# Performance work log

Hardware: AMD Instinct MI355X
Metric: run time of the kernel (lower is better)

## Reference

```python
import jax, jax.numpy as jnp
import numpy as np

D_MODEL = 1024
NUM_HEADS = 16
WINDOW = 128
DEPTH = D_MODEL // NUM_HEADS


def setup_inputs() -> dict:
    key = jax.random.key(0)
    ks = jax.random.split(key, 9)
    B, S = 2, 2048
    scale = 1.0 / np.sqrt(D_MODEL)
    x = jax.random.normal(ks[0], (B, S, D_MODEL), dtype=jnp.float32)
    Wq = jax.random.normal(ks[1], (D_MODEL, D_MODEL), dtype=jnp.float32) * scale
    Wk = jax.random.normal(ks[2], (D_MODEL, D_MODEL), dtype=jnp.float32) * scale
    Wv = jax.random.normal(ks[3], (D_MODEL, D_MODEL), dtype=jnp.float32) * scale
    Wo = jax.random.normal(ks[4], (D_MODEL, D_MODEL), dtype=jnp.float32) * scale
    bq = jnp.zeros((D_MODEL,), jnp.float32)
    bk = jnp.zeros((D_MODEL,), jnp.float32)
    bv = jnp.zeros((D_MODEL,), jnp.float32)
    bo = jnp.zeros((D_MODEL,), jnp.float32)
    return {"x": x, "Wq": Wq, "bq": bq, "Wk": Wk, "bk": bk,
            "Wv": Wv, "bv": bv, "Wo": Wo, "bo": bo}


def _split_heads(t, B, S):
    # [B,S,D] -> [B,H,S,depth]
    return t.reshape(B, S, NUM_HEADS, DEPTH).transpose(0, 2, 1, 3)


def reference(x, Wq, bq, Wk, bk, Wv, bv, Wo, bo):
    B, S, _ = x.shape
    q = _split_heads(x @ Wq + bq, B, S)
    k = _split_heads(x @ Wk + bk, B, S)
    v = _split_heads(x @ Wv + bv, B, S)
    scores = jnp.einsum('bhqd,bhkd->bhqk', q, k) / jnp.sqrt(jnp.float32(DEPTH))
    idx = jnp.arange(S)
    # mask[i_row=j, i_col=i] per original: |i - j| <= window (symmetric)
    local = jnp.abs(idx[None, :] - idx[:, None]) <= WINDOW  # [S,S]
    scores = jnp.where(local[None, None], scores, jnp.float32(-1e9))
    attn = jax.nn.softmax(scores, axis=-1)
    out = jnp.einsum('bhqk,bhkd->bhqd', attn, v)
    concat = out.transpose(0, 2, 1, 3).reshape(B, S, D_MODEL)
    return concat @ Wo + bo
```

## Files before the change

kernel.cpp:

```cpp
#include <hip/hip_runtime.h>
#include <cstdint>
#include <cstddef>

typedef __attribute__((ext_vector_type(8))) short short8;
typedef __attribute__((ext_vector_type(4))) short short4v;
typedef __attribute__((ext_vector_type(4))) float f32x4;
typedef short8 bf16x8;

typedef __attribute__((address_space(1))) const unsigned GU;
typedef __attribute__((address_space(3))) unsigned LU;

__device__ __forceinline__ short f2bf(float f) {
  unsigned u = __builtin_bit_cast(unsigned, f);
  u += 0x7fffu + ((u >> 16) & 1u);
  return (short)(u >> 16);
}

__global__ __launch_bounds__(256) void k_prep(const float* __restrict__ x,
                                              const float* __restrict__ W0, const float* __restrict__ W1,
                                              const float* __restrict__ W2, const float* __restrict__ W3,
                                              short* __restrict__ xb, short* __restrict__ WT) {
  __shared__ short T[64 * 72];
  int bid = blockIdx.x;
  int tid = threadIdx.x;
  if (bid < 2048) {
    size_t i = ((size_t)bid * 256 + tid) * 8;
    f32x4 a = *(const f32x4*)(x + i);
    f32x4 b = *(const f32x4*)(x + i + 4);
    short8 o;
#pragma unroll
    for (int j = 0; j < 4; ++j) { o[j] = f2bf(a[j]); o[4 + j] = f2bf(b[j]); }
    *(short8*)(xb + i) = o;
    return;
  }
  bid -= 2048;
  int widx = bid >> 8;
  int t = bid & 255;
  int kr = (t >> 4) * 64, nc = (t & 15) * 64;
  const float* W = widx == 0 ? W0 : widx == 1 ? W1 : widx == 2 ? W2 : W3;
  short* out = WT + (size_t)widx * 1048576;
#pragma unroll
  for (int i = 0; i < 4; ++i) {
    int idx = tid + i * 256;
    int k = idx >> 4, n4 = (idx & 15) << 2;
    f32x4 v = *(const f32x4*)(W + (size_t)(kr + k) * 1024 + nc + n4);
#pragma unroll
    for (int j = 0; j < 4; ++j) T[(n4 + j) * 72 + k] = f2bf(v[j]);
  }
  __syncthreads();
#pragma unroll
  for (int i = 0; i < 2; ++i) {
    int idx = tid + i * 256;
    int n = idx >> 3, k8 = (idx & 7) << 3;
    *(short8*)(out + (size_t)(nc + n) * 1024 + kr + k8) = *(const short8*)&T[n * 72 + k8];
  }
}

__global__ __launch_bounds__(512, 1) void k_gemm256(
    const short* __restrict__ A, const short* __restrict__ BT,
    const float* __restrict__ bias0, const float* __restrict__ bias1, const float* __restrict__ bias2,
    short* __restrict__ outb) {
  __shared__ short S[73728];
  const int tid = threadIdx.x;
  const int lane = tid & 63, w = tid >> 6;
  const int g = lane >> 4, qi = lane & 15;
  const int wm = w >> 2, wn = w & 3;
  int bid = blockIdx.x;
  int xcd = bid & 7, ii = bid >> 3;
  const int tm = (xcd >> 1) * 4 + (ii >> 3);
  const int tn = (xcd & 1) * 8 + (ii & 7);
  const int m0 = tm * 256, n0 = tn * 192;
  const size_t K = 1024;
  const short* Ab = A + (size_t)m0 * K;
  const short* Bb = BT + (size_t)n0 * K;

  auto stage64 = [&](int roff, const short* gbase, int kt) {
    int r = tid >> 3;
    int js = ((tid & 7) ^ (r & 7)) << 3;
    __builtin_amdgcn_global_load_lds((GU*)(gbase + (size_t)r * K + kt * 64 + js),
                                     (LU*)(&S[roff + tid * 8]), 16, 0, 0);
  };
  auto lda_a = [&](int abase, int mf, int kk) -> bf16x8 {
    int row = (mf & 3) * 16 + qi;
    int reg = wm * 2 + (mf >> 2);
    return *(const bf16x8*)&S[abase + reg * 4096 + row * 64 + (((kk * 4 + g) ^ (row & 7)) << 3)];
  };
  auto lda_b = [&](int bbase, int nf, int kk) -> bf16x8 {
    int c = wn * 48 + nf * 16 + qi;
    int reg = c >> 6, row = c & 63;
    return *(const bf16x8*)&S[bbase + reg * 4096 + row * 64 + (((kk * 4 + g) ^ (row & 7)) << 3)];
  };

  f32x4 acc[8][3];
#pragma unroll
  for (int i = 0; i < 8; ++i)
#pragma unroll
    for (int j = 0; j < 3; ++j) acc[i][j] = (f32x4)(0.0f);

#define MFA(mi, ni, av, bv) \
  acc[mi][ni] = __builtin_amdgcn_mfma_f32_16x16x32_bf16(av, bv, acc[mi][ni], 0, 0, 0)
#define MF12(Aa, Bb_, o) \
  MFA((o)+0,0,(Aa)[(o)+0],(Bb_)[0]); MFA((o)+0,1,(Aa)[(o)+0],(Bb_)[1]); MFA((o)+0,2,(Aa)[(o)+0],(Bb_)[2]); \
  MFA((o)+1,0,(Aa)[(o)+1],(Bb_)[0]); MFA((o)+1,1,(Aa)[(o)+1],(Bb_)[1]); MFA((o)+1,2,(Aa)[(o)+1],(Bb_)[2]); \
  MFA((o)+2,0,(Aa)[(o)+2],(Bb_)[0]); MFA((o)+2,1,(Aa)[(o)+2],(Bb_)[1]); MFA((o)+2,2,(Aa)[(o)+2],(Bb_)[2]); \
  MFA((o)+3,0,(Aa)[(o)+3],(Bb_)[0]); MFA((o)+3,1,(Aa)[(o)+3],(Bb_)[1]); MFA((o)+3,2,(Aa)[(o)+3],(Bb_)[2])
#define SB __builtin_amdgcn_sched_barrier(0)
#define PHASE_TAIL(MFMAS) do { \
    SB; \
    __builtin_amdgcn_s_barrier(); \
    asm volatile("s_waitcnt lgkmcnt(0)" ::: "memory"); \
    SB; \
    __builtin_amdgcn_s_setprio(1); \
    MFMAS; \
    __builtin_amdgcn_s_setprio(0); \
    SB; \
    __builtin_amdgcn_s_barrier(); \
  } while (0)

  stage64(0,             Ab,            0);
  stage64(4096,          Ab + 65536,    0);
  stage64(8192,          Ab + 131072,   0);
  stage64(12288,         Ab + 196608,   0);
  stage64(49152,         Bb,            0);
  stage64(49152 + 4096,  Bb + 65536,    0);
  stage64(49152 + 8192,  Bb + 131072,   0);
  stage64(16384,         Ab,            1);
  stage64(16384 + 4096,  Ab + 65536,    1);
  stage64(16384 + 8192,  Ab + 131072,   1);
  stage64(16384 + 12288, Ab + 196608,   1);
  stage64(61440,         Bb,            1);
  stage64(61440 + 4096,  Bb + 65536,    1);
  stage64(61440 + 8192,  Bb + 131072,   1);
  asm volatile("s_waitcnt vmcnt(7)" ::: "memory");
  __builtin_amdgcn_s_barrier();

  for (int t = 0; t < 16; ++t) {
    const int rA = (t % 3) * 16384;
    const int a2 = ((t + 2) % 3) * 16384;
    const int rB = 49152 + (t & 1) * 12288;
    const int t2 = t + 2 < 15 ? t + 2 : 15;
    bf16x8 aA[8], aB[3], cA[8], cB[3];

#pragma unroll
    for (int mf = 0; mf < 4; ++mf) aA[mf] = lda_a(rA, mf, 0);
#pragma unroll
    for (int nf = 0; nf < 3; ++nf) aB[nf] = lda_b(rB, nf, 0);
    stage64(a2,        Ab,         t2);
    stage64(a2 + 4096, Ab + 65536, t2);
    PHASE_TAIL(MF12(aA, aB, 0));
#pragma unroll
    for (int mf = 4; mf < 8; ++mf) aA[mf] = lda_a(rA, mf, 0);
#pragma unroll
    for (int nf = 0; nf < 3; ++nf) cB[nf] = lda_b(rB, nf, 1);
    stage64(a2 + 8192,  Ab + 131072, t2);
    stage64(a2 + 12288, Ab + 196608, t2);
    PHASE_TAIL(MF12(aA, aB, 4));
#pragma unroll
    for (int mf = 0; mf < 4; ++mf) cA[mf] = lda_a(rA, mf, 1);
    stage64(rB,        Bb,         t2);
    stage64(rB + 4096, Bb + 65536, t2);
    PHASE_TAIL(MF12(cA, cB, 0));
#pragma unroll
    for (int mf = 4; mf < 8; ++mf) cA[mf] = lda_a(rA, mf, 1);
    stage64(rB + 8192, Bb + 131072, t2);
    asm volatile("s_waitcnt vmcnt(7)" ::: "memory");
    PHASE_TAIL(MF12(cA, cB, 4));
  }
#undef PHASE_TAIL
#undef MF12
#undef MFA
#undef SB

  asm volatile("s_waitcnt vmcnt(0)" ::: "memory");
  __syncthreads();
  float bv[3];
#pragma unroll
  for (int nf = 0; nf < 3; ++nf) {
    int colg = n0 + wn * 48 + nf * 16 + qi;
    int sel = colg >> 10;
    const float* bias = sel == 0 ? bias0 : (sel == 1 ? bias1 : bias2);
    bv[nf] = bias[colg & 1023];
  }
  short* Ep = S;
#pragma unroll
  for (int p = 0; p < 2; ++p) {
    __syncthreads();
    if (wm == p) {
#pragma unroll
      for (int mf = 0; mf < 8; ++mf)
#pragma unroll
        for (int nf = 0; nf < 3; ++nf)
#pragma unroll
          for (int j = 0; j < 4; ++j)
            Ep[(mf * 16 + g * 4 + j) * 200 + wn * 48 + nf * 16 + qi] =
                f2bf(acc[mf][nf][j] + bv[nf]);
    }
    __syncthreads();
#pragma unroll
    for (int i = 0; i < 6; ++i) {
      int idx = tid + i * 512;
      int r = idx / 24, c8 = (idx % 24) * 8;
      int grow = m0 + p * 128 + r;
      int colg = n0 + c8;
      int sel = colg >> 10;
      *(short8*)&outb[(size_t)sel * 4194304 + (size_t)grow * 1024 + (colg & 1023)] =
          *(const short8*)&Ep[r * 200 + c8];
    }
  }
}

__global__ __launch_bounds__(256, 2) void k_gemmO(
    const short* __restrict__ A, const short* __restrict__ BT,
    const float* __restrict__ bias0, float* __restrict__ outf) {
  __shared__ short Smem[16384];
  const int tid = threadIdx.x;
  const int lane = tid & 63, w = tid >> 6;
  const int g = lane >> 4, qi = lane & 15;
  const int wr = (w >> 1) * 64, wc = (w & 1) * 64;
  int bid = blockIdx.x;
  int xcd = bid & 7, ii = bid >> 3;
  const int tm = (xcd >> 1) * 8 + (ii >> 2);
  const int tn = (xcd & 1) * 4 + (ii & 3);
  const int m0 = tm * 128, n0 = tn * 128;
  const size_t K = 1024;
  const short* Ab = A + (size_t)m0 * K;
  const short* Bb = BT + (size_t)n0 * K;

  auto stage = [&](int buf, int k0) {
    short* Asb = Smem + buf * 4096;
    short* Bsb = Smem + 8192 + buf * 4096;
#pragma unroll
    for (int i = 0; i < 2; ++i) {
      int cidx = tid + i * 256;
      int r = cidx >> 2;
      int csw = ((cidx & 3) ^ ((r >> 1) & 3)) << 3;
      __builtin_amdgcn_global_load_lds((GU*)(Ab + (size_t)r * K + k0 + csw),
                                       (LU*)(&Asb[cidx * 8]), 16, 0, 0);
      __builtin_amdgcn_global_load_lds((GU*)(Bb + (size_t)r * K + k0 + csw),
                                       (LU*)(&Bsb[cidx * 8]), 16, 0, 0);
    }
  };

  f32x4 acc[4][4];
#pragma unroll
  for (int i = 0; i < 4; ++i)
#pragma unroll
    for (int j = 0; j < 4; ++j) acc[i][j] = (f32x4)(0.0f);

  stage(0, 0);
  __syncthreads();
  for (int kt = 0; kt < 32; ++kt) {
    int cur = kt & 1;
    if (kt < 31) stage(cur ^ 1, (kt + 1) * 32);
    const short* Asb = Smem + cur * 4096;
    const short* Bsb = Smem + 8192 + cur * 4096;
    bf16x8 a[4], b[4];
#pragma unroll
    for (int mf = 0; mf < 4; ++mf) {
      int R = wr + mf * 16 + qi;
      a[mf] = *(const bf16x8*)&Asb[R * 32 + ((g ^ ((R >> 1) & 3)) << 3)];
    }
#pragma unroll
    for (int nf = 0; nf < 4; ++nf) {
      int R = wc + nf * 16 + qi;
      b[nf] = *(const bf16x8*)&Bsb[R * 32 + ((g ^ ((R >> 1) & 3)) << 3)];
    }
#pragma unroll
    for (int mf = 0; mf < 4; ++mf)
#pragma unroll
      for (int nf = 0; nf < 4; ++nf)
        acc[mf][nf] = __builtin_amdgcn_mfma_f32_16x16x32_bf16(a[mf], b[nf], acc[mf][nf], 0, 0, 0);
    __syncthreads();
  }

  float* Ft = (float*)Smem;
  float bv[4];
#pragma unroll
  for (int nf = 0; nf < 4; ++nf) bv[nf] = bias0[n0 + wc + nf * 16 + qi];
#pragma unroll
  for (int mf = 0; mf < 4; ++mf) {
    __syncthreads();
#pragma unroll
    for (int nf = 0; nf < 4; ++nf)
#pragma unroll
      for (int j = 0; j < 4; ++j)
        Ft[((w >> 1) * 16 + g * 4 + j) * 136 + wc + nf * 16 + qi] = acc[mf][nf][j] + bv[nf];
    __syncthreads();
#pragma unroll
    for (int i = 0; i < 4; ++i) {
      int idx = tid + i * 256;
      int r = idx >> 5, c4 = (idx & 31) << 2;
      int row = m0 + ((r >> 4) << 6) + mf * 16 + (r & 15);
      *(f32x4*)&outf[(size_t)row * 1024 + n0 + c4] = *(const f32x4*)&Ft[r * 136 + c4];
    }
  }
}

__global__ __launch_bounds__(256, 2) void k_attn(const short* __restrict__ qg_,
                                                 const short* __restrict__ kg_,
                                                 const short* __restrict__ vg_,
                                                 short* __restrict__ outp) {
  __shared__ short Qs[64 * 72];
  __shared__ short Ks[64 * 72];
  __shared__ short Vs[64 * 72];
  __shared__ short Ps[4][16 * 72];
  int bid = blockIdx.x;
  int qt = bid & 31, h = (bid >> 5) & 15, b = bid >> 9;
  int q0 = qt * 64;
  int tid = threadIdx.x, lane = tid & 63, w = tid >> 6;
  int g = lane >> 4, qi = lane & 15;

  const short* qsrc = qg_ + ((size_t)b * 2048 + q0) * 1024 + h * 64;
#pragma unroll
  for (int i = 0; i < 2; ++i) {
    int idx = tid + i * 256;
    int r = idx >> 3, c = (idx & 7) << 3;
    *(short8*)&Qs[r * 72 + c] = *(const short8*)&qsrc[(size_t)r * 1024 + c];
  }
  __syncthreads();
  bf16x8 qf0 = *(const bf16x8*)&Qs[(w * 16 + qi) * 72 + g * 8];
  bf16x8 qf1 = *(const bf16x8*)&Qs[(w * 16 + qi) * 72 + 32 + g * 8];

  float m = -1e30f, l = 0.f;
  f32x4 oacc[4];
#pragma unroll
  for (int i = 0; i < 4; ++i) oacc[i] = (f32x4)(0.0f);
  int qglob = q0 + w * 16 + qi;

  for (int cc = 0; cc < 5; ++cc) {
    int kb0 = q0 - 128 + cc * 64;
    if (kb0 < 0 || kb0 >= 2048) continue;
    __syncthreads();
    const short* ksrc = kg_ + ((size_t)b * 2048 + kb0) * 1024 + h * 64;
    const short* vsrc = vg_ + ((size_t)b * 2048 + kb0) * 1024 + h * 64;
#pragma unroll
    for (int i = 0; i < 2; ++i) {
      int idx = tid + i * 256;
      int r = idx >> 3, c = (idx & 7) << 3;
      *(short8*)&Ks[r * 72 + c] = *(const short8*)&ksrc[(size_t)r * 1024 + c];
      short8 vv = *(const short8*)&vsrc[(size_t)r * 1024 + c];
#pragma unroll
      for (int j = 0; j < 8; ++j) {
        int d = c + j;
        Vs[d * 72 + ((r + ((d >> 3) << 3)) & 63)] = vv[j];
      }
    }
    __syncthreads();

    f32x4 st[4];
#pragma unroll
    for (int i = 0; i < 4; ++i) st[i] = (f32x4)(0.0f);
#pragma unroll
    for (int mf = 0; mf < 4; ++mf) {
      bf16x8 kf0 = *(const bf16x8*)&Ks[(mf * 16 + qi) * 72 + g * 8];
      bf16x8 kf1 = *(const bf16x8*)&Ks[(mf * 16 + qi) * 72 + 32 + g * 8];
      st[mf] = __builtin_amdgcn_mfma_f32_16x16x32_bf16(kf0, qf0, st[mf], 0, 0, 0);
      st[mf] = __builtin_amdgcn_mfma_f32_16x16x32_bf16(kf1, qf1, st[mf], 0, 0, 0);
    }

    float pv[16];
    float pm = -1e30f;
    if (cc >= 1 && cc <= 3) {
#pragma unroll
      for (int mf = 0; mf < 4; ++mf)
#pragma unroll
        for (int j = 0; j < 4; ++j) {
          float s = st[mf][j] * 0.125f;
          pv[mf * 4 + j] = s;
          pm = fmaxf(pm, s);
        }
    } else {
#pragma unroll
      for (int mf = 0; mf < 4; ++mf)
#pragma unroll
        for (int j = 0; j < 4; ++j) {
          int kcol = kb0 + mf * 16 + g * 4 + j;
          float s = st[mf][j] * 0.125f;
          int d = kcol - qglob;
          bool valid = (d >= -128) && (d <= 128);
          s = valid ? s : -1e30f;
          pv[mf * 4 + j] = s;
          pm = fmaxf(pm, s);
        }
    }
    pm = fmaxf(pm, __shfl_xor(pm, 16));
    pm = fmaxf(pm, __shfl_xor(pm, 32));
    float mnew = fmaxf(m, pm);
    float scale = __expf(m - mnew);
    float ls = 0.f;
#pragma unroll
    for (int e = 0; e < 16; ++e) {
      float p = pv[e] > -1e29f ? __expf(pv[e] - mnew) : 0.f;
      pv[e] = p;
      ls += p;
    }
    ls += __shfl_xor(ls, 16);
    ls += __shfl_xor(ls, 32);
    l = l * scale + ls;
    m = mnew;
#pragma unroll
    for (int mf = 0; mf < 4; ++mf) oacc[mf] *= scale;

#pragma unroll
    for (int f = 0; f < 4; ++f) {
      short4v pk;
#pragma unroll
      for (int j = 0; j < 4; ++j) pk[j] = f2bf(pv[f * 4 + j]);
      *(short4v*)&Ps[w][qi * 72 + f * 16 + g * 4] = pk;
    }

#pragma unroll
    for (int ks = 0; ks < 2; ++ks) {
      bf16x8 pf = *(const bf16x8*)&Ps[w][qi * 72 + ks * 32 + g * 8];
#pragma unroll
      for (int mf = 0; mf < 4; ++mf) {
        int dd = mf * 16 + qi;
        int pc = ((ks * 32 + g * 8) + ((dd >> 3) << 3)) & 63;
        bf16x8 vf = *(const bf16x8*)&Vs[dd * 72 + pc];
        oacc[mf] = __builtin_amdgcn_mfma_f32_16x16x32_bf16(vf, pf, oacc[mf], 0, 0, 0);
      }
    }
  }

  __syncthreads();
  short* Os = Ks;
  float inv = 1.f / l;
#pragma unroll
  for (int mf = 0; mf < 4; ++mf) {
    short4v pk;
#pragma unroll
    for (int j = 0; j < 4; ++j) pk[j] = f2bf(oacc[mf][j] * inv);
    *(short4v*)&Os[(w * 16 + qi) * 72 + mf * 16 + g * 4] = pk;
  }
  __syncthreads();
  short* dst = outp + ((size_t)b * 2048 + q0) * 1024 + h * 64;
  int r = tid >> 2, c16 = (tid & 3) << 4;
  *(short8*)&dst[(size_t)r * 1024 + c16] = *(const short8*)&Os[r * 72 + c16];
  *(short8*)&dst[(size_t)r * 1024 + c16 + 8] = *(const short8*)&Os[r * 72 + c16 + 8];
}

extern "C" void kernel_launch(void* const* d_in, const int* in_sizes, int n_in,
                              void* d_out, int out_size, void* d_ws, size_t ws_size,
                              hipStream_t stream) {
  const float* x  = (const float*)d_in[0];
  const float* Wq = (const float*)d_in[1];
  const float* bq = (const float*)d_in[2];
  const float* Wk = (const float*)d_in[3];
  const float* bk = (const float*)d_in[4];
  const float* Wv = (const float*)d_in[5];
  const float* bv = (const float*)d_in[6];
  const float* Wo = (const float*)d_in[7];
  const float* bo = (const float*)d_in[8];

  short* ws = (short*)d_ws;
  short* xb       = ws;
  short* qkv      = ws + 4194304;
  short* vbuf     = qkv + 2 * 4194304;
  short* attn_out = ws;
  short* WT       = ws + 4 * 4194304;

  k_prep<<<3072, 256, 0, stream>>>(x, Wq, Wk, Wv, Wo, xb, WT);
  k_gemm256<<<256, 512, 0, stream>>>(xb, WT, bq, bk, bv, qkv);
  k_attn<<<1024, 256, 0, stream>>>(qkv, qkv + 4194304, vbuf, attn_out);
  k_gemmO<<<256, 256, 0, stream>>>(attn_out, WT + 3 * 1048576, bo, (float*)d_out);
}
```

Measured before the change: 82.24 us.

## Halve QKV GEMM M-tile to 128 and double-buffer with 512 blocks

The fused QKV projection GEMM tile shrinks from 256x192 to 128x192, the grid doubles to 512 blocks, LDS drops to about 80KB, and launch bounds allow several blocks per CU. The triple-buffered A / double-buffered B prefetch becomes a simpler double buffer with a full vmcnt(0) wait each iteration. The goal is more blocks in flight to fill all CUs and to hide latency through occupancy. The costs are lower arithmetic intensity per tile, more global traffic for B, and less prefetch depth, since each iteration now waits for all loads.

```diff
diff --git a/kernel.cpp b/kernel.cpp
--- a/kernel.cpp
+++ b/kernel.cpp
@@ -56,20 +56,20 @@
   }
 }
 
-__global__ __launch_bounds__(512, 1) void k_gemm256(
+__global__ __launch_bounds__(512, 4) void k_gemm256(
     const short* __restrict__ A, const short* __restrict__ BT,
     const float* __restrict__ bias0, const float* __restrict__ bias1, const float* __restrict__ bias2,
     short* __restrict__ outb) {
-  __shared__ short S[73728];
+  __shared__ short S[40960];
   const int tid = threadIdx.x;
   const int lane = tid & 63, w = tid >> 6;
   const int g = lane >> 4, qi = lane & 15;
   const int wm = w >> 2, wn = w & 3;
   int bid = blockIdx.x;
   int xcd = bid & 7, ii = bid >> 3;
-  const int tm = (xcd >> 1) * 4 + (ii >> 3);
+  const int tm = (xcd >> 1) * 8 + (ii >> 3);
   const int tn = (xcd & 1) * 8 + (ii & 7);
-  const int m0 = tm * 256, n0 = tn * 192;
+  const int m0 = tm * 128, n0 = tn * 192;
   const size_t K = 1024;
   const short* Ab = A + (size_t)m0 * K;
   const short* Bb = BT + (size_t)n0 * K;
@@ -81,9 +81,8 @@
                                      (LU*)(&S[roff + tid * 8]), 16, 0, 0);
   };
   auto lda_a = [&](int abase, int mf, int kk) -> bf16x8 {
-    int row = (mf & 3) * 16 + qi;
-    int reg = wm * 2 + (mf >> 2);
-    return *(const bf16x8*)&S[abase + reg * 4096 + row * 64 + (((kk * 4 + g) ^ (row & 7)) << 3)];
+    int row = mf * 16 + qi;
+    return *(const bf16x8*)&S[abase + wm * 4096 + row * 64 + (((kk * 4 + g) ^ (row & 7)) << 3)];
   };
   auto lda_b = [&](int bbase, int nf, int kk) -> bf16x8 {
     int c = wn * 48 + nf * 16 + qi;
@@ -91,19 +90,17 @@
     return *(const bf16x8*)&S[bbase + reg * 4096 + row * 64 + (((kk * 4 + g) ^ (row & 7)) << 3)];
   };
 
-  f32x4 acc[8][3];
-#pragma unroll
-  for (int i = 0; i < 8; ++i)
+  f32x4 acc[4][3];
+#pragma unroll
+  for (int i = 0; i < 4; ++i)
 #pragma unroll
     for (int j = 0; j < 3; ++j) acc[i][j] = (f32x4)(0.0f);
 
 #define MFA(mi, ni, av, bv) \
   acc[mi][ni] = __builtin_amdgcn_mfma_f32_16x16x32_bf16(av, bv, acc[mi][ni], 0, 0, 0)
-#define MF12(Aa, Bb_, o) \
+#define MF6(Aa, Bb_, o) \
   MFA((o)+0,0,(Aa)[(o)+0],(Bb_)[0]); MFA((o)+0,1,(Aa)[(o)+0],(Bb_)[1]); MFA((o)+0,2,(Aa)[(o)+0],(Bb_)[2]); \
-  MFA((o)+1,0,(Aa)[(o)+1],(Bb_)[0]); MFA((o)+1,1,(Aa)[(o)+1],(Bb_)[1]); MFA((o)+1,2,(Aa)[(o)+1],(Bb_)[2]); \
-  MFA((o)+2,0,(Aa)[(o)+2],(Bb_)[0]); MFA((o)+2,1,(Aa)[(o)+2],(Bb_)[1]); MFA((o)+2,2,(Aa)[(o)+2],(Bb_)[2]); \
-  MFA((o)+3,0,(Aa)[(o)+3],(Bb_)[0]); MFA((o)+3,1,(Aa)[(o)+3],(Bb_)[1]); MFA((o)+3,2,(Aa)[(o)+3],(Bb_)[2])
+  MFA((o)+1,0,(Aa)[(o)+1],(Bb_)[0]); MFA((o)+1,1,(Aa)[(o)+1],(Bb_)[1]); MFA((o)+1,2,(Aa)[(o)+1],(Bb_)[2])
 #define SB __builtin_amdgcn_sched_barrier(0)
 #define PHASE_TAIL(MFMAS) do { \
     SB; \
@@ -117,57 +114,42 @@
     __builtin_amdgcn_s_barrier(); \
   } while (0)
 
-  stage64(0,             Ab,            0);
-  stage64(4096,          Ab + 65536,    0);
-  stage64(8192,          Ab + 131072,   0);
-  stage64(12288,         Ab + 196608,   0);
-  stage64(49152,         Bb,            0);
-  stage64(49152 + 4096,  Bb + 65536,    0);
-  stage64(49152 + 8192,  Bb + 131072,   0);
-  stage64(16384,         Ab,            1);
-  stage64(16384 + 4096,  Ab + 65536,    1);
-  stage64(16384 + 8192,  Ab + 131072,   1);
-  stage64(16384 + 12288, Ab + 196608,   1);
-  stage64(61440,         Bb,            1);
-  stage64(61440 + 4096,  Bb + 65536,    1);
-  stage64(61440 + 8192,  Bb + 131072,   1);
-  asm volatile("s_waitcnt vmcnt(7)" ::: "memory");
+  stage64(0,             Ab,          0);
+  stage64(4096,          Ab + 65536,  0);
+  stage64(16384,         Bb,          0);
+  stage64(16384 + 4096,  Bb + 65536,  0);
+  stage64(16384 + 8192,  Bb + 131072, 0);
+  asm volatile("s_waitcnt vmcnt(0)" ::: "memory");
   __builtin_amdgcn_s_barrier();
 
   for (int t = 0; t < 16; ++t) {
-    const int rA = (t % 3) * 16384;
-    const int a2 = ((t + 2) % 3) * 16384;
-    const int rB = 49152 + (t & 1) * 12288;
-    const int t2 = t + 2 < 15 ? t + 2 : 15;
-    bf16x8 aA[8], aB[3], cA[8], cB[3];
+    const int rA = (t & 1) * 8192, nA = rA ^ 8192;
+    const int rB = 16384 + (t & 1) * 12288;
+    const int nB = 16384 + ((t + 1) & 1) * 12288;
+    const int t1 = t + 1 < 15 ? t + 1 : 15;
+    bf16x8 aA[4], aB[3], cA[4], cB[3];
 
 #pragma unroll
     for (int mf = 0; mf < 4; ++mf) aA[mf] = lda_a(rA, mf, 0);
 #pragma unroll
     for (int nf = 0; nf < 3; ++nf) aB[nf] = lda_b(rB, nf, 0);
-    stage64(a2,        Ab,         t2);
-    stage64(a2 + 4096, Ab + 65536, t2);
-    PHASE_TAIL(MF12(aA, aB, 0));
-#pragma unroll
-    for (int mf = 4; mf < 8; ++mf) aA[mf] = lda_a(rA, mf, 0);
+    stage64(nA, Ab, t1);
+    stage64(nB, Bb, t1);
+    PHASE_TAIL(MF6(aA, aB, 0));
+#pragma unroll
+    for (int mf = 0; mf < 4; ++mf) cA[mf] = lda_a(rA, mf, 1);
 #pragma unroll
     for (int nf = 0; nf < 3; ++nf) cB[nf] = lda_b(rB, nf, 1);
-    stage64(a2 + 8192,  Ab + 131072, t2);
-    stage64(a2 + 12288, Ab + 196608, t2);
-    PHASE_TAIL(MF12(aA, aB, 4));
-#pragma unroll
-    for (int mf = 0; mf < 4; ++mf) cA[mf] = lda_a(rA, mf, 1);
-    stage64(rB,        Bb,         t2);
-    stage64(rB + 4096, Bb + 65536, t2);
-    PHASE_TAIL(MF12(cA, cB, 0));
-#pragma unroll
-    for (int mf = 4; mf < 8; ++mf) cA[mf] = lda_a(rA, mf, 1);
-    stage64(rB + 8192, Bb + 131072, t2);
-    asm volatile("s_waitcnt vmcnt(7)" ::: "memory");
-    PHASE_TAIL(MF12(cA, cB, 4));
+    stage64(nA + 4096, Ab + 65536, t1);
+    stage64(nB + 4096, Bb + 65536, t1);
+    PHASE_TAIL(MF6(aA, aB, 2));
+    stage64(nB + 8192, Bb + 131072, t1);
+    PHASE_TAIL(MF6(cA, cB, 0));
+    asm volatile("s_waitcnt vmcnt(0)" ::: "memory");
+    PHASE_TAIL(MF6(cA, cB, 2));
   }
 #undef PHASE_TAIL
-#undef MF12
+#undef MF6
 #undef MFA
 #undef SB
 
@@ -183,29 +165,23 @@
   }
   short* Ep = S;
 #pragma unroll
-  for (int p = 0; p < 2; ++p) {
-    __syncthreads();
-    if (wm == p) {
-#pragma unroll
-      for (int mf = 0; mf < 8; ++mf)
-#pragma unroll
-        for (int nf = 0; nf < 3; ++nf)
-#pragma unroll
-          for (int j = 0; j < 4; ++j)
-            Ep[(mf * 16 + g * 4 + j) * 200 + wn * 48 + nf * 16 + qi] =
-                f2bf(acc[mf][nf][j] + bv[nf]);
-    }
-    __syncthreads();
-#pragma unroll
-    for (int i = 0; i < 6; ++i) {
-      int idx = tid + i * 512;
-      int r = idx / 24, c8 = (idx % 24) * 8;
-      int grow = m0 + p * 128 + r;
-      int colg = n0 + c8;
-      int sel = colg >> 10;
-      *(short8*)&outb[(size_t)sel * 4194304 + (size_t)grow * 1024 + (colg & 1023)] =
-          *(const short8*)&Ep[r * 200 + c8];
-    }
+  for (int mf = 0; mf < 4; ++mf)
+#pragma unroll
+    for (int nf = 0; nf < 3; ++nf)
+#pragma unroll
+      for (int j = 0; j < 4; ++j)
+        Ep[(wm * 64 + mf * 16 + g * 4 + j) * 200 + wn * 48 + nf * 16 + qi] =
+            f2bf(acc[mf][nf][j] + bv[nf]);
+  __syncthreads();
+#pragma unroll
+  for (int i = 0; i < 6; ++i) {
+    int idx = tid + i * 512;
+    int r = idx / 24, c8 = (idx % 24) * 8;
+    int grow = m0 + r;
+    int colg = n0 + c8;
+    int sel = colg >> 10;
+    *(short8*)&outb[(size_t)sel * 4194304 + (size_t)grow * 1024 + (colg & 1023)] =
+        *(const short8*)&Ep[r * 200 + c8];
   }
 }
 
@@ -460,7 +436,7 @@
   short* WT       = ws + 4 * 4194304;
 
   k_prep<<<3072, 256, 0, stream>>>(x, Wq, Wk, Wv, Wo, xb, WT);
-  k_gemm256<<<256, 512, 0, stream>>>(xb, WT, bq, bk, bv, qkv);
+  k_gemm256<<<512, 512, 0, stream>>>(xb, WT, bq, bk, bv, qkv);
   k_attn<<<1024, 256, 0, stream>>>(qkv, qkv + 4194304, vbuf, attn_out);
   k_gemmO<<<256, 256, 0, stream>>>(attn_out, WT + 3 * 1048576, bo, (float*)d_out);
 }
```

Measured after the change: 83.47 us. No clear change (+1.5%).
